# Performance work log

Hardware: AMD Instinct MI355X
Metric: run time of the kernel (lower is better)

## Reference

```python
import jax, jax.numpy as jnp
import numpy as np

N_NODES = 100000
N_EDGES = 1600000
IN = 128
OUT = 32
HEADS = 4
NEG_SLOPE = 0.2


def setup_inputs() -> dict:
    key = jax.random.key(0)
    ks = jax.random.split(key, 6)
    x = jax.random.normal(ks[0], (N_NODES, IN), dtype=jnp.float32)
    row = jax.random.randint(ks[1], (N_EDGES,), 0, N_NODES, dtype=jnp.int32)
    col = jax.random.randint(ks[2], (N_EDGES,), 0, N_NODES, dtype=jnp.int32)
    W = jax.random.normal(ks[3], (OUT * HEADS, IN), dtype=jnp.float32) * (1.0 / np.sqrt(IN))
    b = jnp.zeros((OUT * HEADS,), dtype=jnp.float32)
    a_l = jax.random.normal(ks[4], (1, OUT, HEADS), dtype=jnp.float32) * 0.1
    a_r = jax.random.normal(ks[5], (1, OUT, HEADS), dtype=jnp.float32) * 0.1
    return {"x": x, "row": row, "col": col, "W": W, "b": b, "a_l": a_l, "a_r": a_r}


def reference(x, row, col, W, b, a_l, a_r):
    N = x.shape[0]
    # Z: [N, OUT, HEADS] (row-major view of [N, OUT*HEADS], matching torch .view)
    Z = (x @ W.T + b).reshape(N, OUT, HEADS)
    e_l = jnp.sum(Z * a_l, axis=1)  # [N, HEADS]
    e_r = jnp.sum(Z * a_r, axis=1)  # [N, HEADS]
    e = e_l[row] + e_r[col]         # [E, HEADS]
    e = jnp.where(e > 0, e, NEG_SLOPE * e)  # LeakyReLU
    # segment softmax over edges grouped by destination (row)
    m = jax.ops.segment_max(e, row, num_segments=N)      # [N, HEADS]
    ex = jnp.exp(e - m[row])                              # [E, HEADS]
    denom = jax.ops.segment_sum(ex, row, num_segments=N)  # [N, HEADS]
    alpha = ex / denom[row]                               # [E, HEADS]
    # bspmm: out[i,:,h] = sum_{(i,j) in E} alpha[e,h] * Z[j,:,h]
    out = jax.ops.segment_sum(alpha[:, None, :] * Z[col], row, num_segments=N)
    return out
```

## Files before the change

### kernel.cpp

```cpp
#include <hip/hip_runtime.h>
#include <hip/hip_bf16.h>
#include <math.h>


typedef __attribute__((ext_vector_type(8))) short bf16x8;
typedef __attribute__((ext_vector_type(4))) float f32x4;

__device__ __forceinline__ ushort f2bf(float f) {
  __hip_bfloat16 h = __float2bfloat16(f);
  return __builtin_bit_cast(ushort, h);
}
__device__ __forceinline__ float bf2f(ushort u) {
  unsigned v = ((unsigned)u) << 16;
  return __builtin_bit_cast(float, v);
}

__global__ __launch_bounds__(256, 2) void gemm_z(
    const float* __restrict__ x, const float* __restrict__ W,
    const float* __restrict__ bias, ushort* __restrict__ Zh, int N) {
  __shared__ ushort xh[64 * 128];
  __shared__ ushort xl[64 * 128];
  const int t = threadIdx.x;
  const int lane = t & 63;
  const int wv = t >> 6;
  const int row0 = blockIdx.x * 64;
  const int l15 = lane & 15, l4 = lane >> 4;

  bf16x8 Bh[2][4], Bl[2][4];
#pragma unroll
  for (int ct = 0; ct < 2; ++ct) {
    int ch = wv * 32 + ct * 16 + l15;
#pragma unroll
    for (int kf = 0; kf < 4; ++kf) {
      int k0 = kf * 32 + l4 * 8;
      const float* wp = W + (size_t)ch * 128 + k0;
      float4 w0 = *(const float4*)(wp);
      float4 w1 = *(const float4*)(wp + 4);
      float wf[8] = {w0.x, w0.y, w0.z, w0.w, w1.x, w1.y, w1.z, w1.w};
      bf16x8 hi, lo;
#pragma unroll
      for (int j = 0; j < 8; ++j) {
        ushort hb = f2bf(wf[j]);
        hi[j] = (short)hb;
        lo[j] = (short)f2bf(wf[j] - bf2f(hb));
      }
      Bh[ct][kf] = hi;
      Bl[ct][kf] = lo;
    }
  }

#pragma unroll
  for (int i = 0; i < 8; ++i) {
    int f4 = i * 256 + t;
    int r = f4 >> 5;
    int k = (f4 & 31) * 4;
    int gr = row0 + r;
    float4 v = make_float4(0.f, 0.f, 0.f, 0.f);
    if (gr < N) v = ((const float4*)x)[(size_t)gr * 32 + (f4 & 31)];
    float vf[4] = {v.x, v.y, v.z, v.w};
    ushort hs[4], ls[4];
#pragma unroll
    for (int j = 0; j < 4; ++j) {
      hs[j] = f2bf(vf[j]);
      ls[j] = f2bf(vf[j] - bf2f(hs[j]));
    }
    int idx = r * 128 + (k ^ ((r & 7) << 3));
    uint2 hv, lv;
    hv.x = hs[0] | ((unsigned)hs[1] << 16);
    hv.y = hs[2] | ((unsigned)hs[3] << 16);
    lv.x = ls[0] | ((unsigned)ls[1] << 16);
    lv.y = ls[2] | ((unsigned)ls[3] << 16);
    *(uint2*)&xh[idx] = hv;
    *(uint2*)&xl[idx] = lv;
  }
  __syncthreads();

  f32x4 acc[4][2];
#pragma unroll
  for (int rt = 0; rt < 4; ++rt)
#pragma unroll
    for (int ct = 0; ct < 2; ++ct) acc[rt][ct] = (f32x4){0.f, 0.f, 0.f, 0.f};

#pragma unroll
  for (int kf = 0; kf < 4; ++kf) {
#pragma unroll
    for (int rt = 0; rt < 4; ++rt) {
      int r = rt * 16 + l15;
      int k = kf * 32 + l4 * 8;
      int idx = r * 128 + (k ^ ((r & 7) << 3));
      bf16x8 ah = *(const bf16x8*)&xh[idx];
      bf16x8 al = *(const bf16x8*)&xl[idx];
#pragma unroll
      for (int ct = 0; ct < 2; ++ct) {
        acc[rt][ct] = __builtin_amdgcn_mfma_f32_16x16x32_bf16(ah, Bh[ct][kf], acc[rt][ct], 0, 0, 0);
        acc[rt][ct] = __builtin_amdgcn_mfma_f32_16x16x32_bf16(al, Bh[ct][kf], acc[rt][ct], 0, 0, 0);
        acc[rt][ct] = __builtin_amdgcn_mfma_f32_16x16x32_bf16(ah, Bl[ct][kf], acc[rt][ct], 0, 0, 0);
      }
    }
  }

  float bv[2];
  bv[0] = bias[wv * 32 + l15];
  bv[1] = bias[wv * 32 + 16 + l15];
#pragma unroll
  for (int rt = 0; rt < 4; ++rt) {
#pragma unroll
    for (int ct = 0; ct < 2; ++ct) {
      int ch = wv * 32 + ct * 16 + l15;
      unsigned zc = (unsigned)((ch & 3) * 32 + (ch >> 2));
#pragma unroll
      for (int j = 0; j < 4; ++j) {
        int r = row0 + rt * 16 + l4 * 4 + j;
        if (r < N) {
          float v = acc[rt][ct][j] + bv[ct];
          Zh[(unsigned)r * 128 + zc] = f2bf(v);
        }
      }
    }
  }
}

__global__ __launch_bounds__(256) void node_e(
    const ushort* __restrict__ Zh, const float* __restrict__ a_l,
    const float* __restrict__ a_r, float* __restrict__ el,
    float* __restrict__ er, int N4) {
  __shared__ float sal[128], sar[128];
  int t = threadIdx.x;
  if (t < 128) { sal[t] = a_l[t]; sar[t] = a_r[t]; }
  __syncthreads();
  int idx = blockIdx.x * 256 + t;
  if (idx >= N4) return;
  int n = idx >> 2, h = idx & 3;
  const ushort* zp = Zh + (unsigned)n * 128 + h * 32;
  float sl = 0.f, sr = 0.f;
#pragma unroll
  for (int q = 0; q < 8; ++q) {
    uint2 zz = *(const uint2*)&zp[q * 4];
    float z0 = bf2f((ushort)(zz.x & 0xffff));
    float z1 = bf2f((ushort)(zz.x >> 16));
    float z2 = bf2f((ushort)(zz.y & 0xffff));
    float z3 = bf2f((ushort)(zz.y >> 16));
    int o = q * 4;
    sl += z0 * sal[(o + 0) * 4 + h] + z1 * sal[(o + 1) * 4 + h]
        + z2 * sal[(o + 2) * 4 + h] + z3 * sal[(o + 3) * 4 + h];
    sr += z0 * sar[(o + 0) * 4 + h] + z1 * sar[(o + 1) * 4 + h]
        + z2 * sar[(o + 2) * 4 + h] + z3 * sar[(o + 3) * 4 + h];
  }
  el[idx] = sl;
  er[idx] = sr;
}

__global__ __launch_bounds__(256) void deg_cnt(
    const int* __restrict__ row, int* __restrict__ deg,
    int* __restrict__ rank, int E) {
  int e = blockIdx.x * 256 + threadIdx.x;
  if (e < E) rank[e] = atomicAdd(&deg[row[e]], 1);
}

__global__ __launch_bounds__(256) void scan1(
    const int* __restrict__ deg, int* __restrict__ base,
    int* __restrict__ bsum, int N) {
  __shared__ int s[256];
  int i = blockIdx.x * 256 + threadIdx.x;
  int v = (i < N) ? deg[i] : 0;
  s[threadIdx.x] = v;
  __syncthreads();
#pragma unroll
  for (int off = 1; off < 256; off <<= 1) {
    int t = (threadIdx.x >= off) ? s[threadIdx.x - off] : 0;
    __syncthreads();
    s[threadIdx.x] += t;
    __syncthreads();
  }
  if (i < N) base[i] = s[threadIdx.x] - v;
  if (threadIdx.x == 255) bsum[blockIdx.x] = s[255];
}

__global__ __launch_bounds__(512) void scan2(int* __restrict__ bsum, int NB) {
  __shared__ int s[512];
  int v = (threadIdx.x < NB) ? bsum[threadIdx.x] : 0;
  s[threadIdx.x] = v;
  __syncthreads();
#pragma unroll
  for (int off = 1; off < 512; off <<= 1) {
    int t = (threadIdx.x >= off) ? s[threadIdx.x - off] : 0;
    __syncthreads();
    s[threadIdx.x] += t;
    __syncthreads();
  }
  if (threadIdx.x < NB) bsum[threadIdx.x] = s[threadIdx.x] - v;
}

__global__ __launch_bounds__(256) void fill(
    const int* __restrict__ row, const int* __restrict__ col,
    const int* __restrict__ rank, const int* __restrict__ base,
    const int* __restrict__ bsum, int* __restrict__ sorted_col, int E) {
  int e = blockIdx.x * 256 + threadIdx.x;
  if (e < E) {
    int r = row[e];
    sorted_col[base[r] + bsum[r >> 8] + rank[e]] = col[e];
  }
}

__global__ __launch_bounds__(256) void gather(
    const int* __restrict__ base, const int* __restrict__ bsum,
    const int* __restrict__ deg, const int* __restrict__ sorted_col,
    const float* __restrict__ el, const float* __restrict__ er,
    const ushort* __restrict__ Zh, float* __restrict__ out, int N) {
  int t = threadIdx.x;
  int lane = t & 63;
  int n = blockIdx.x * 4 + (t >> 6);
  if (n >= N) return;
  int h = lane >> 4;
  int o0 = (lane & 15) << 1;
  int s = base[n] + bsum[n >> 8];
  int d = deg[n];
  float elv = el[(unsigned)(n << 2) + h];
  unsigned zoff = (unsigned)(h * 32 + o0);
  float acc0 = 0.f, acc1 = 0.f, sum = 0.f;
#pragma unroll 4
  for (int p = s; p < s + d; ++p) {
    int cl = sorted_col[p];
    float e = elv + er[((unsigned)cl << 2) + h];
    e = fmaxf(e, 0.2f * e);
    float xv = __expf(e);
    unsigned zz = *(const unsigned*)&Zh[((unsigned)cl << 7) + zoff];
    acc0 = fmaf(xv, bf2f((ushort)(zz & 0xffff)), acc0);
    acc1 = fmaf(xv, bf2f((ushort)(zz >> 16)), acc1);
    sum += xv;
  }
  float inv = (d > 0) ? 1.0f / sum : 0.f;
  unsigned ob = ((unsigned)n << 7) + (unsigned)(o0 << 2) + h;
  out[ob] = acc0 * inv;
  out[ob + 4] = acc1 * inv;
}

extern "C" void kernel_launch(void* const* d_in, const int* in_sizes, int n_in,
                              void* d_out, int out_size, void* d_ws, size_t ws_size,
                              hipStream_t stream) {
  const float* x   = (const float*)d_in[0];
  const int*   row = (const int*)d_in[1];
  const int*   col = (const int*)d_in[2];
  const float* W   = (const float*)d_in[3];
  const float* b   = (const float*)d_in[4];
  const float* a_l = (const float*)d_in[5];
  const float* a_r = (const float*)d_in[6];
  float* out = (float*)d_out;

  const int N = in_sizes[0] / 128;
  const int E = in_sizes[1];
  const int NB = (N + 255) / 256;

  char* w = (char*)d_ws;
  ushort* Zh       = (ushort*)w;             w += (size_t)N * 128 * 2;
  int*   sorted_col= (int*)w;                w += (size_t)E * 4;
  int*   rank      = (int*)w;                w += (size_t)E * 4;
  float* el        = (float*)w;              w += (size_t)N * 4 * 4;
  float* er        = (float*)w;              w += (size_t)N * 4 * 4;
  int*   deg       = (int*)w;                w += (size_t)N * 4;
  int*   base      = (int*)w;                w += (size_t)N * 4;
  int*   bsum      = (int*)w;                w += 512 * 4;

  hipMemsetAsync(deg, 0, (size_t)N * sizeof(int), stream);

  gemm_z<<<(N + 63) / 64, 256, 0, stream>>>(x, W, b, Zh, N);
  node_e<<<(N * 4 + 255) / 256, 256, 0, stream>>>(Zh, a_l, a_r, el, er, N * 4);
  deg_cnt<<<(E + 255) / 256, 256, 0, stream>>>(row, deg, rank, E);
  scan1<<<NB, 256, 0, stream>>>(deg, base, bsum, N);
  scan2<<<1, 512, 0, stream>>>(bsum, NB);
  fill<<<(E + 255) / 256, 256, 0, stream>>>(row, col, rank, base, bsum,
                                            sorted_col, E);
  gather<<<(N + 3) / 4, 256, 0, stream>>>(base, bsum, deg, sorted_col, el, er,
                                          Zh, out, N);
}
```

Measured before the change: 233.6 us.

## Fuse independent kernels horizontally and batch edge-weight computation in gather

The GEMM and degree-count kernels are merged into one launch by block-index ranges, and so are the node attention-score and first scan kernels. This cuts launch count and lets the independent work run concurrently. The gather loop now has 16 lanes per head each compute one edge's exp weight and column index, then broadcasts them with ds_bpermute. This removes redundant per-lane exp and er loads, at the cost of a wave reduction for the sum and extra permute instructions.

```diff
diff --git a/kernel.cpp b/kernel.cpp
--- a/kernel.cpp
+++ b/kernel.cpp
@@ -15,11 +15,20 @@
   return __builtin_bit_cast(float, v);
 }
 
-__global__ __launch_bounds__(256, 2) void gemm_z(
+__global__ __launch_bounds__(256, 2) void gemm_deg(
     const float* __restrict__ x, const float* __restrict__ W,
-    const float* __restrict__ bias, ushort* __restrict__ Zh, int N) {
+    const float* __restrict__ bias, ushort* __restrict__ Zh, int N,
+    const int* __restrict__ row, int* __restrict__ deg,
+    int* __restrict__ rank, int E, int G1) {
   __shared__ ushort xh[64 * 128];
   __shared__ ushort xl[64 * 128];
+
+  if ((int)blockIdx.x >= G1) {
+    int e = ((int)blockIdx.x - G1) * 256 + threadIdx.x;
+    if (e < E) rank[e] = atomicAdd(&deg[row[e]], 1);
+    return;
+  }
+
   const int t = threadIdx.x;
   const int lane = t & 63;
   const int wv = t >> 6;
@@ -120,60 +129,55 @@
   }
 }
 
-__global__ __launch_bounds__(256) void node_e(
+__global__ __launch_bounds__(256) void node_scan(
     const ushort* __restrict__ Zh, const float* __restrict__ a_l,
     const float* __restrict__ a_r, float* __restrict__ el,
-    float* __restrict__ er, int N4) {
+    float* __restrict__ er, int N4,
+    const int* __restrict__ deg, int* __restrict__ basev,
+    int* __restrict__ bsum, int N, int G1) {
   __shared__ float sal[128], sar[128];
+  __shared__ int ss[256];
   int t = threadIdx.x;
-  if (t < 128) { sal[t] = a_l[t]; sar[t] = a_r[t]; }
-  __syncthreads();
-  int idx = blockIdx.x * 256 + t;
-  if (idx >= N4) return;
-  int n = idx >> 2, h = idx & 3;
-  const ushort* zp = Zh + (unsigned)n * 128 + h * 32;
-  float sl = 0.f, sr = 0.f;
-#pragma unroll
-  for (int q = 0; q < 8; ++q) {
-    uint2 zz = *(const uint2*)&zp[q * 4];
-    float z0 = bf2f((ushort)(zz.x & 0xffff));
-    float z1 = bf2f((ushort)(zz.x >> 16));
-    float z2 = bf2f((ushort)(zz.y & 0xffff));
-    float z3 = bf2f((ushort)(zz.y >> 16));
-    int o = q * 4;
-    sl += z0 * sal[(o + 0) * 4 + h] + z1 * sal[(o + 1) * 4 + h]
-        + z2 * sal[(o + 2) * 4 + h] + z3 * sal[(o + 3) * 4 + h];
-    sr += z0 * sar[(o + 0) * 4 + h] + z1 * sar[(o + 1) * 4 + h]
-        + z2 * sar[(o + 2) * 4 + h] + z3 * sar[(o + 3) * 4 + h];
-  }
-  el[idx] = sl;
-  er[idx] = sr;
-}
-
-__global__ __launch_bounds__(256) void deg_cnt(
-    const int* __restrict__ row, int* __restrict__ deg,
-    int* __restrict__ rank, int E) {
-  int e = blockIdx.x * 256 + threadIdx.x;
-  if (e < E) rank[e] = atomicAdd(&deg[row[e]], 1);
-}
-
-__global__ __launch_bounds__(256) void scan1(
-    const int* __restrict__ deg, int* __restrict__ base,
-    int* __restrict__ bsum, int N) {
-  __shared__ int s[256];
-  int i = blockIdx.x * 256 + threadIdx.x;
-  int v = (i < N) ? deg[i] : 0;
-  s[threadIdx.x] = v;
-  __syncthreads();
-#pragma unroll
-  for (int off = 1; off < 256; off <<= 1) {
-    int t = (threadIdx.x >= off) ? s[threadIdx.x - off] : 0;
+
+  if ((int)blockIdx.x < G1) {
+    if (t < 128) { sal[t] = a_l[t]; sar[t] = a_r[t]; }
     __syncthreads();
-    s[threadIdx.x] += t;
+    int idx = blockIdx.x * 256 + t;
+    if (idx >= N4) return;
+    int n = idx >> 2, h = idx & 3;
+    const ushort* zp = Zh + (unsigned)n * 128 + h * 32;
+    float sl = 0.f, sr = 0.f;
+#pragma unroll
+    for (int q = 0; q < 8; ++q) {
+      uint2 zz = *(const uint2*)&zp[q * 4];
+      float z0 = bf2f((ushort)(zz.x & 0xffff));
+      float z1 = bf2f((ushort)(zz.x >> 16));
+      float z2 = bf2f((ushort)(zz.y & 0xffff));
+      float z3 = bf2f((ushort)(zz.y >> 16));
+      int o = q * 4;
+      sl += z0 * sal[(o + 0) * 4 + h] + z1 * sal[(o + 1) * 4 + h]
+          + z2 * sal[(o + 2) * 4 + h] + z3 * sal[(o + 3) * 4 + h];
+      sr += z0 * sar[(o + 0) * 4 + h] + z1 * sar[(o + 1) * 4 + h]
+          + z2 * sar[(o + 2) * 4 + h] + z3 * sar[(o + 3) * 4 + h];
+    }
+    el[idx] = sl;
+    er[idx] = sr;
+  } else {
+    int bid = (int)blockIdx.x - G1;
+    int i = bid * 256 + t;
+    int v = (i < N) ? deg[i] : 0;
+    ss[t] = v;
     __syncthreads();
-  }
-  if (i < N) base[i] = s[threadIdx.x] - v;
-  if (threadIdx.x == 255) bsum[blockIdx.x] = s[255];
+#pragma unroll
+    for (int off = 1; off < 256; off <<= 1) {
+      int u = (t >= off) ? ss[t - off] : 0;
+      __syncthreads();
+      ss[t] += u;
+      __syncthreads();
+    }
+    if (i < N) basev[i] = ss[t] - v;
+    if (t == 255) bsum[bid] = ss[255];
+  }
 }
 
 __global__ __launch_bounds__(512) void scan2(int* __restrict__ bsum, int NB) {
@@ -212,25 +216,46 @@
   int n = blockIdx.x * 4 + (t >> 6);
   if (n >= N) return;
   int h = lane >> 4;
-  int o0 = (lane & 15) << 1;
+  int j = lane & 15;
   int s = base[n] + bsum[n >> 8];
   int d = deg[n];
-  float elv = el[(unsigned)(n << 2) + h];
-  unsigned zoff = (unsigned)(h * 32 + o0);
-  float acc0 = 0.f, acc1 = 0.f, sum = 0.f;
-#pragma unroll 4
-  for (int p = s; p < s + d; ++p) {
-    int cl = sorted_col[p];
-    float e = elv + er[((unsigned)cl << 2) + h];
-    e = fmaxf(e, 0.2f * e);
-    float xv = __expf(e);
-    unsigned zz = *(const unsigned*)&Zh[((unsigned)cl << 7) + zoff];
-    acc0 = fmaf(xv, bf2f((ushort)(zz & 0xffff)), acc0);
-    acc1 = fmaf(xv, bf2f((ushort)(zz >> 16)), acc1);
-    sum += xv;
-  }
+  int end = s + d;
+  float elv = el[((unsigned)n << 2) + h];
+  float acc0 = 0.f, acc1 = 0.f, sumA = 0.f;
+  const unsigned* Zh32 = (const unsigned*)Zh;
+  const unsigned zlane = (unsigned)lane;
+  const int bpb = (lane & 48) << 2;
+
+  for (int p = s; p < end; p += 16) {
+    int cnt = end - p;
+    if (cnt > 16) cnt = 16;
+    int cl = 0;
+    float xv = 0.f;
+    if (j < cnt) {
+      cl = sorted_col[p + j];
+      float e = elv + er[((unsigned)cl << 2) + h];
+      e = fmaxf(e, 0.2f * e);
+      xv = __expf(e);
+    }
+    sumA += xv;
+    for (int jj = 0; jj < cnt; ++jj) {
+      int a = bpb + (jj << 2);
+      float xvb = __builtin_bit_cast(float,
+          __builtin_amdgcn_ds_bpermute(a, __builtin_bit_cast(int, xv)));
+      unsigned clb = (unsigned)__builtin_amdgcn_ds_bpermute(a, cl);
+      unsigned zz = Zh32[(clb << 6) + zlane];
+      acc0 = fmaf(xvb, __builtin_bit_cast(float, zz << 16), acc0);
+      acc1 = fmaf(xvb, __builtin_bit_cast(float, zz & 0xffff0000u), acc1);
+    }
+  }
+  float sum = sumA;
+  sum += __shfl_xor(sum, 1, 64);
+  sum += __shfl_xor(sum, 2, 64);
+  sum += __shfl_xor(sum, 4, 64);
+  sum += __shfl_xor(sum, 8, 64);
   float inv = (d > 0) ? 1.0f / sum : 0.f;
-  unsigned ob = ((unsigned)n << 7) + (unsigned)(o0 << 2) + h;
+  unsigned o0 = (unsigned)(j << 1);
+  unsigned ob = ((unsigned)n << 7) + (o0 << 2) + (unsigned)h;
   out[ob] = acc0 * inv;
   out[ob + 4] = acc1 * inv;
 }
@@ -263,10 +288,13 @@
 
   hipMemsetAsync(deg, 0, (size_t)N * sizeof(int), stream);
 
-  gemm_z<<<(N + 63) / 64, 256, 0, stream>>>(x, W, b, Zh, N);
-  node_e<<<(N * 4 + 255) / 256, 256, 0, stream>>>(Zh, a_l, a_r, el, er, N * 4);
-  deg_cnt<<<(E + 255) / 256, 256, 0, stream>>>(row, deg, rank, E);
-  scan1<<<NB, 256, 0, stream>>>(deg, base, bsum, N);
+  const int G1g = (N + 63) / 64;
+  const int G2d = (E + 255) / 256;
+  gemm_deg<<<G1g + G2d, 256, 0, stream>>>(x, W, b, Zh, N, row, deg, rank, E, G1g);
+
+  const int G1n = (N * 4 + 255) / 256;
+  node_scan<<<G1n + NB, 256, 0, stream>>>(Zh, a_l, a_r, el, er, N * 4,
+                                          deg, base, bsum, N, G1n);
   scan2<<<1, 512, 0, stream>>>(bsum, NB);
   fill<<<(E + 255) / 256, 256, 0, stream>>>(row, col, rank, base, bsum,
                                             sorted_col, E);
```

New measurement: 256.7 us. 9.9% more time.
